# Performance work log

Hardware: AMD Instinct MI355X
Metric: run time of the kernel (lower is better)

## Reference

```python
import jax, jax.numpy as jnp
import numpy as np
from jax import lax

# ---- module config (matches init_kwargs) ----
TARGET_H, TARGET_W = 1024, 1024
SMOOTH_K = 3
DIL_K = 3
DIL_ITERS = 2
DIL_BETA = 5.0
DIL_STRENGTH = 1.0


def _cubic_weights(t):
    """Keys cubic convolution weights (a=-0.75, torch bicubic). t: [N] frac in [0,1). -> [N,4] for taps at offsets -1,0,1,2."""
    a = -0.75
    t1 = t + 1.0  # distance of tap -1
    w0 = a * t1**3 - 5.0 * a * t1**2 + 8.0 * a * t1 - 4.0 * a
    w1 = (a + 2.0) * t**3 - (a + 3.0) * t**2 + 1.0
    u = 1.0 - t
    w2 = (a + 2.0) * u**3 - (a + 3.0) * u**2 + 1.0
    u2 = 2.0 - t
    w3 = a * u2**3 - 5.0 * a * u2**2 + 8.0 * a * u2 - 4.0 * a
    return jnp.stack([w0, w1, w2, w3], axis=-1)


def _taps(n_in, n_out):
    # grid_sample with align_corners=True over a full linspace(-1,1) grid maps
    # output pixel j -> input coord linspace(0, n_in-1, n_out)[j]
    src = jnp.linspace(0.0, n_in - 1.0, n_out)
    i0 = jnp.floor(src)
    t = src - i0
    idx = (i0[:, None] + jnp.arange(-1, 3)[None, :]).astype(jnp.int32)
    idx = jnp.clip(idx, 0, n_in - 1)  # padding_mode='border'
    return idx, _cubic_weights(t)


def _resize_bicubic(x, ht, wt):
    B, C, H, W = x.shape
    ih, wh = _taps(H, ht)
    iw, ww = _taps(W, wt)
    # rows: [B,C,ht,4,W] -> weighted sum over taps
    xr = x[:, :, ih, :]
    xr = jnp.einsum('bcthw,th->bctw', xr.transpose(0, 1, 2, 4, 3), wh) if False else (xr * wh[None, None, :, :, None]).sum(axis=3)
    # cols: [B,C,ht,wt,4]
    xc = xr[:, :, :, iw]
    return (xc * ww[None, None, None, :, :]).sum(axis=-1)


def _gaussian_kernel(k):
    sigma = k / 3.0
    r = np.arange(k, dtype=np.float32) - k // 2
    k1 = np.exp(-0.5 * (r / sigma) ** 2)
    k1 = k1 / k1.sum()
    k2 = np.outer(k1, k1)
    return jnp.asarray(k2.reshape(1, 1, k, k))


def _smooth(x):
    kern = _gaussian_kernel(SMOOTH_K)
    pad = SMOOTH_K // 2
    return lax.conv_general_dilated(
        x, kern, window_strides=(1, 1), padding=[(pad, pad), (pad, pad)],
        dimension_numbers=('NCHW', 'OIHW', 'NCHW'))


def _soft_dilate(x):
    # windowed logsumexp: lse = (1/beta) * log sum_window exp(beta * x),
    # with zero padding inside the window (matches F.unfold padding).
    p = DIL_K // 2
    for _ in range(DIL_ITERS):
        xp = jnp.pad(x, ((0, 0), (0, 0), (p, p), (p, p)))
        e = jnp.exp(DIL_BETA * (xp - 1.0))  # shift by 1.0 (x in [0,1]) for stability
        s = lax.reduce_window(e, 0.0, lax.add, (1, 1, DIL_K, DIL_K), (1, 1, 1, 1), 'VALID')
        x = jnp.clip(1.0 + jnp.log(s) / DIL_BETA, 0.0, 1.0)
    return x  # DIL_STRENGTH == 1.0 -> no blend with original


def setup_inputs() -> dict:
    key = jax.random.key(0)
    detris_output = jax.random.normal(key, (8, 1, 256, 256), dtype=jnp.float32)
    return {"detris_output": detris_output}


def reference(detris_output) -> jnp.ndarray:
    x = jax.nn.sigmoid(detris_output)
    x = _resize_bicubic(x, TARGET_H, TARGET_W)
    x = _smooth(x)
    x = _soft_dilate(x)
    return x
```

## Files before the change

kernel.cpp:

```cpp
#include <hip/hip_runtime.h>
#include <hip/hip_fp16.h>

#define B_ 8
#define HI 256
#define WI 256
#define HO 1024
#define WO 1024

#define TLE 64
#define NRS 24
#define SSTR 25
#define HS 18
#define EW 38
#define SC (255.0f / 1023.0f)
#define F5L2E 7.2134752f
#define EXPM5 0.0067379470f
#define GW0 0.27406862f
#define GW1 0.45186276f
#define C02 0.13862944f

__device__ __forceinline__ int basef(int g) {
    int yc = min(max(g, 0), HO - 1);
    return (int)floorf((float)yc * SC) - 2;
}

__device__ __forceinline__ void tap6(int g, int* base_out, float w[6]) {
    int yc = min(max(g, 0), HO - 1);
    int base = basef(g);
#pragma unroll
    for (int s = 0; s < 6; ++s) w[s] = 0.0f;
    if (g >= 0 && g < HO) {
#pragma unroll
        for (int d = -1; d <= 1; ++d) {
            int yd = yc + d;
            if (yd < 0 || yd >= HO) continue;
            float src = (float)yd * SC;
            float fi0 = floorf(src);
            float tt = src - fi0;
            const float a = -0.75f;
            float t1 = tt + 1.0f;
            float c0 = ((a * t1 - 5.0f * a) * t1 + 8.0f * a) * t1 - 4.0f * a;
            float c1 = ((a + 2.0f) * tt - (a + 3.0f)) * tt * tt + 1.0f;
            float u = 1.0f - tt;
            float c2 = ((a + 2.0f) * u - (a + 3.0f)) * u * u + 1.0f;
            float u2 = 2.0f - tt;
            float c3 = ((a * u2 - 5.0f * a) * u2 + 8.0f * a) * u2 - 4.0f * a;
            int s0 = ((int)fi0 - 1) - base;
            float gg = (d == 0) ? GW1 : GW0;
            w[s0 + 0] += gg * c0;
            w[s0 + 1] += gg * c1;
            w[s0 + 2] += gg * c2;
            w[s0 + 3] += gg * c3;
        }
    }
    *base_out = base;
}

__device__ __forceinline__ void pad8(const float w[6], int d, float scl, float w8[8]) {
#pragma unroll
    for (int j = 0; j < 8; ++j) {
        float a = (j < 6) ? w[j] : 0.0f;
        float bq = (j >= 1 && j < 7) ? w[j - 1] : 0.0f;
        w8[j] = ((d == 0) ? a : bq) * scl;
    }
}

__device__ __forceinline__ __half2 hmin2(__half2 a, __half2 b) {
    unsigned int ua = __builtin_bit_cast(unsigned int, a);
    unsigned int ub = __builtin_bit_cast(unsigned int, b);
    unsigned int r;
    asm("v_pk_min_f16 %0, %1, %2" : "=v"(r) : "v"(ua), "v"(ub));
    return __builtin_bit_cast(__half2, r);
}

__global__ __launch_bounds__(256, 7) void k_fused(const float* __restrict__ in,
                                                  float* __restrict__ out) {
    __shared__ __align__(16) unsigned int Eu[68 * EW];
    __shared__ float4 Hs[NRS * HS];
    __shared__ float4 xAw[72], xBw[72];
    __shared__ float4 vAw[70], vBw[70];
    __shared__ int vgb[14], xgb[18];
    float* SL = (float*)Eu;

    const int tid = threadIdx.x;
    const int bx = blockIdx.x, by = blockIdx.y, b = blockIdx.z;
    const int gy0 = by * TLE, gx0 = bx * TLE;
    const int rlo = basef(gy0 - 3);
    const int clo = basef(gx0 - 4);

    const float* pin = in + b * (HI * WI);
    float g0, g1, g2 = 0.0f;
    {
        int i0 = tid, i1 = tid + 256;
        int r0 = i0 / NRS, c0 = i0 - r0 * NRS;
        int r1 = i1 / NRS, c1 = i1 - r1 * NRS;
        g0 = pin[min(max(rlo + r0, 0), HI - 1) * WI + min(max(clo + c0, 0), HI - 1)];
        g1 = pin[min(max(rlo + r1, 0), HI - 1) * WI + min(max(clo + c1, 0), HI - 1)];
        if (tid < 64) {
            int i2 = tid + 512;
            int r2 = i2 / NRS, c2 = i2 - r2 * NRS;
            g2 = pin[min(max(rlo + r2, 0), HI - 1) * WI + min(max(clo + c2, 0), HI - 1)];
        }
    }

    if (tid < 70) {
        int fy = tid + 1;
        int base; float w[6];
        tap6(gy0 + fy - 3, &base, w);
        int q = tid / 5;
        int bs = basef(gy0 + (1 + 5 * q) - 3);
        float w8[8];
        pad8(w, base - bs, F5L2E, w8);
        vAw[tid] = make_float4(w8[0], w8[1], w8[2], w8[3]);
        vBw[tid] = make_float4(w8[4], w8[5], w8[6], w8[7]);
    } else if (tid < 84) {
        vgb[tid - 70] = basef(gy0 + (1 + 5 * (tid - 70)) - 3);
    } else if (tid < 102) {
        xgb[tid - 84] = basef(gx0 + 4 * (tid - 84) - 4);
    } else if (tid >= 128 && tid < 200) {
        int xe = tid - 128;
        int base; float w[6];
        tap6(gx0 + xe - 4, &base, w);
        int bs = basef(gx0 + (xe & ~3) - 4);
        float w8[8];
        pad8(w, base - bs, 1.0f, w8);
        xAw[xe] = make_float4(w8[0], w8[1], w8[2], w8[3]);
        xBw[xe] = make_float4(w8[4], w8[5], w8[6], w8[7]);
    }

    {
        int i0 = tid, i1 = tid + 256;
        int r0 = i0 / NRS, c0 = i0 - r0 * NRS;
        int r1 = i1 / NRS, c1 = i1 - r1 * NRS;
        SL[r0 * SSTR + c0] = 1.0f / (1.0f + __expf(-g0));
        SL[r1 * SSTR + c1] = 1.0f / (1.0f + __expf(-g1));
        if (tid < 64) {
            int i2 = tid + 512;
            int r2 = i2 / NRS, c2 = i2 - r2 * NRS;
            SL[r2 * SSTR + c2] = 1.0f / (1.0f + __expf(-g2));
        }
    }
    __syncthreads();

    const int ty = tid / HS;
    const int tx = tid - ty * HS;

    if (tid < 252) {
        int cbg = xgb[tx] - clo;
        int wc[8];
#pragma unroll
        for (int j = 0; j < 8; ++j) wc[j] = min(cbg + j, NRS - 1);
        float xw0[8], xw1[8], xw2[8], xw3[8];
        {
            int xe0 = tx << 2;
            float4 a0 = xAw[xe0 + 0], b0 = xBw[xe0 + 0];
            float4 a1 = xAw[xe0 + 1], b1 = xBw[xe0 + 1];
            float4 a2 = xAw[xe0 + 2], b2 = xBw[xe0 + 2];
            float4 a3 = xAw[xe0 + 3], b3 = xBw[xe0 + 3];
            xw0[0]=a0.x; xw0[1]=a0.y; xw0[2]=a0.z; xw0[3]=a0.w; xw0[4]=b0.x; xw0[5]=b0.y; xw0[6]=b0.z; xw0[7]=b0.w;
            xw1[0]=a1.x; xw1[1]=a1.y; xw1[2]=a1.z; xw1[3]=a1.w; xw1[4]=b1.x; xw1[5]=b1.y; xw1[6]=b1.z; xw1[7]=b1.w;
            xw2[0]=a2.x; xw2[1]=a2.y; xw2[2]=a2.z; xw2[3]=a2.w; xw2[4]=b2.x; xw2[5]=b2.y; xw2[6]=b2.z; xw2[7]=b2.w;
            xw3[0]=a3.x; xw3[1]=a3.y; xw3[2]=a3.z; xw3[3]=a3.w; xw3[4]=b3.x; xw3[5]=b3.y; xw3[6]=b3.z; xw3[7]=b3.w;
        }
        for (int r = ty; r < NRS; r += 14) {
            const float* srow = SL + r * SSTR;
            float wnd[8];
#pragma unroll
            for (int j = 0; j < 8; ++j) wnd[j] = srow[wc[j]];
            float s0 = wnd[0]*xw0[0], s1 = wnd[0]*xw1[0], s2 = wnd[0]*xw2[0], s3 = wnd[0]*xw3[0];
#pragma unroll
            for (int j = 1; j < 8; ++j) {
                s0 = fmaf(wnd[j], xw0[j], s0);
                s1 = fmaf(wnd[j], xw1[j], s1);
                s2 = fmaf(wnd[j], xw2[j], s2);
                s3 = fmaf(wnd[j], xw3[j], s3);
            }
            Hs[r * HS + tx] = make_float4(s0, s1, s2, s3);
        }
    }
    __syncthreads();

    if (tid < 252) {
        const int q = ty;
        const int rbase = vgb[q] - rlo;
        float4 h[8];
#pragma unroll
        for (int i = 0; i < 8; ++i) h[i] = Hs[min(rbase + i, NRS - 1) * HS + tx];
#pragma unroll
        for (int i = 0; i < 5; ++i) {
            int fy = 1 + 5 * q + i;
            if (fy <= 68) {
                float4 wa = vAw[fy - 1], wb = vBw[fy - 1];
                const float wv[8] = {wa.x, wa.y, wa.z, wa.w, wb.x, wb.y, wb.z, wb.w};
                float ax = -F5L2E, ay = -F5L2E, az = -F5L2E, aw = -F5L2E;
#pragma unroll
                for (int j = 0; j < 8; ++j) {
                    ax = fmaf(wv[j], h[j].x, ax);
                    ay = fmaf(wv[j], h[j].y, ay);
                    az = fmaf(wv[j], h[j].z, az);
                    aw = fmaf(wv[j], h[j].w, aw);
                }
                unsigned int p0 = __builtin_bit_cast(unsigned int, __floats2half2_rn(exp2f(ax), exp2f(ay)));
                unsigned int p1 = __builtin_bit_cast(unsigned int, __floats2half2_rn(exp2f(az), exp2f(aw)));
                *reinterpret_cast<uint2*>(&Eu[(fy - 1) * EW + 2 * tx]) = make_uint2(p0, p1);
            }
        }
    }
    __syncthreads();

    {
        const int dx = tid & 15;
        const int sq = tid >> 4;
        const int lr0 = 4 * sq;
        const bool rT = (by == 0)  && (sq == 0);
        const bool rB = (by == 15) && (sq == 15);
        const bool cL = (bx == 0)  && (dx == 0);
        const bool cR = (bx == 15) && (dx == 15);

        const __half2 ONE2 = __floats2half2_rn(1.0f, 1.0f);
        const __half2 EX2  = __floats2half2_rn(EXPM5, EXPM5);
        const unsigned int exu = __builtin_bit_cast(unsigned int, EX2);

        auto H2  = [](unsigned int u) { return __builtin_bit_cast(__half2, u); };
        auto U32 = [](__half2 h) { return __builtin_bit_cast(unsigned int, h); };

        auto HSUM = [&](int lr, __half2 P[3]) {
            const int o = lr * EW + 2 * dx;
            unsigned int a = Eu[o + 1];
            uint2 bc = *reinterpret_cast<const uint2*>(&Eu[o + 2]);
            unsigned int d = Eu[o + 4];
            unsigned int ab  = (a >> 16) | (bc.x << 16);
            unsigned int bcx = (bc.x >> 16) | (bc.y << 16);
            unsigned int cd  = (bc.y >> 16) | (d << 16);
            P[0] = __hadd2(__hadd2(H2(a), H2(ab)), H2(bc.x));
            P[1] = __hadd2(__hadd2(H2(bc.x), H2(bcx)), H2(bc.y));
            P[2] = __hadd2(__hadd2(H2(bc.y), H2(cd)), H2(d));
        };
        auto E2F = [&](const __half2* a, const __half2* bq, const __half2* c,
                       bool rowOv, __half2 Q[2]) {
            __half2 e0 = hmin2(__hadd2(__hadd2(a[0], bq[0]), c[0]), ONE2);
            __half2 e1 = hmin2(__hadd2(__hadd2(a[1], bq[1]), c[1]), ONE2);
            __half2 e2 = hmin2(__hadd2(__hadd2(a[2], bq[2]), c[2]), ONE2);
            if (rowOv) { e0 = EX2; e1 = EX2; e2 = EX2; }
            if (cL) e0 = H2((U32(e0) & 0xFFFF0000u) | (exu & 0x0000FFFFu));
            if (cR) e2 = H2((U32(e2) & 0x0000FFFFu) | (exu & 0xFFFF0000u));
            unsigned int u0 = U32(e0), u1 = U32(e1), u2 = U32(e2);
            unsigned int e01 = (u0 >> 16) | (u1 << 16);
            unsigned int e12 = (u1 >> 16) | (u2 << 16);
            Q[0] = __hadd2(__hadd2(e0, H2(e01)), e1);
            Q[1] = __hadd2(__hadd2(e1, H2(e12)), e2);
        };
        auto OUTF = [&](const __half2* qa, const __half2* qb, const __half2* qc) -> float4 {
            __half2 s0 = __hadd2(__hadd2(qa[0], qb[0]), qc[0]);
            __half2 s1 = __hadd2(__hadd2(qa[1], qb[1]), qc[1]);
            float f0 = __low2float(s0), f1 = __high2float(s0);
            float f2 = __low2float(s1), f3 = __high2float(s1);
            float4 o;
            o.x = fmaxf(fminf(fmaf(C02, __log2f(f0), 1.0f), 1.0f), 0.0f);
            o.y = fmaxf(fminf(fmaf(C02, __log2f(f1), 1.0f), 1.0f), 0.0f);
            o.z = fmaxf(fminf(fmaf(C02, __log2f(f2), 1.0f), 1.0f), 0.0f);
            o.w = fmaxf(fminf(fmaf(C02, __log2f(f3), 1.0f), 1.0f), 0.0f);
            return o;
        };

        __half2 hA[3], hB[3], hC[3], hD[3];
        __half2 eA[2], eB[2], eC[2], eD[2], eE[2], eF[2];
        size_t obase = ((size_t)(b * HO + by * TLE + 4 * sq) * WO) + bx * TLE + (dx << 2);

        HSUM(lr0 + 0, hA); HSUM(lr0 + 1, hB); HSUM(lr0 + 2, hC);
        E2F(hA, hB, hC, rT, eA);
        HSUM(lr0 + 3, hD); E2F(hB, hC, hD, false, eB);
        HSUM(lr0 + 4, hA); E2F(hC, hD, hA, false, eC);
        *reinterpret_cast<float4*>(out + obase) = OUTF(eA, eB, eC); obase += WO;
        HSUM(lr0 + 5, hB); E2F(hD, hA, hB, false, eD);
        *reinterpret_cast<float4*>(out + obase) = OUTF(eB, eC, eD); obase += WO;
        HSUM(lr0 + 6, hC); E2F(hA, hB, hC, false, eE);
        *reinterpret_cast<float4*>(out + obase) = OUTF(eC, eD, eE); obase += WO;
        HSUM(lr0 + 7, hD); E2F(hB, hC, hD, rB, eF);
        *reinterpret_cast<float4*>(out + obase) = OUTF(eD, eE, eF);
    }
}

extern "C" void kernel_launch(void* const* d_in, const int* in_sizes, int n_in,
                              void* d_out, int out_size, void* d_ws, size_t ws_size,
                              hipStream_t stream) {
    const float* in = (const float*)d_in[0];
    float* out = (float*)d_out;
    dim3 g(WO / TLE, HO / TLE, B_);
    k_fused<<<g, dim3(256), 0, stream>>>(in, out);
}
```

Before: 23.35 us.

## Use packed fp16 dot2 for horizontal and vertical resize passes

Converts the resize weights and the intermediate horizontal-pass results to packed fp16 and computes both separable resize passes with v_dot2 fp16 instructions accumulating in fp32. This halves the shared-memory footprint of the weight tables and the intermediate buffer and cuts the FMA count roughly in half. The cost is extra pack and convert instructions and reduced precision of inputs and weights, which could affect accuracy. The exp argument is scaled by about 7.2, which amplifies fp16 rounding.

```diff
diff --git a/kernel.cpp b/kernel.cpp
--- a/kernel.cpp
+++ b/kernel.cpp
@@ -10,7 +10,6 @@
 #define TLE 64
 #define NRS 24
 #define SSTR 25
-#define HS 18
 #define EW 38
 #define SC (255.0f / 1023.0f)
 #define F5L2E 7.2134752f
@@ -18,6 +17,13 @@
 #define GW0 0.27406862f
 #define GW1 0.45186276f
 #define C02 0.13862944f
+
+typedef _Float16 f16x2 __attribute__((ext_vector_type(2)));
+
+__device__ __forceinline__ float dot2(unsigned int a, unsigned int b, float c) {
+    return __builtin_amdgcn_fdot2(__builtin_bit_cast(f16x2, a),
+                                  __builtin_bit_cast(f16x2, b), c, false);
+}
 
 __device__ __forceinline__ int basef(int g) {
     int yc = min(max(g, 0), HO - 1);
@@ -65,6 +71,15 @@
     }
 }
 
+__device__ __forceinline__ uint4 packw8(const float w8[8]) {
+    uint4 r;
+    r.x = __builtin_bit_cast(unsigned int, __floats2half2_rn(w8[0], w8[1]));
+    r.y = __builtin_bit_cast(unsigned int, __floats2half2_rn(w8[2], w8[3]));
+    r.z = __builtin_bit_cast(unsigned int, __floats2half2_rn(w8[4], w8[5]));
+    r.w = __builtin_bit_cast(unsigned int, __floats2half2_rn(w8[6], w8[7]));
+    return r;
+}
+
 __device__ __forceinline__ __half2 hmin2(__half2 a, __half2 b) {
     unsigned int ua = __builtin_bit_cast(unsigned int, a);
     unsigned int ub = __builtin_bit_cast(unsigned int, b);
@@ -76,9 +91,9 @@
 __global__ __launch_bounds__(256, 7) void k_fused(const float* __restrict__ in,
                                                   float* __restrict__ out) {
     __shared__ __align__(16) unsigned int Eu[68 * EW];
-    __shared__ float4 Hs[NRS * HS];
-    __shared__ float4 xAw[72], xBw[72];
-    __shared__ float4 vAw[70], vBw[70];
+    __shared__ __align__(16) unsigned int Hu[NRS * EW];
+    __shared__ uint4 xWu[72];
+    __shared__ uint4 vWu[70];
     __shared__ int vgb[14], xgb[18];
     float* SL = (float*)Eu;
 
@@ -111,8 +126,7 @@
         int bs = basef(gy0 + (1 + 5 * q) - 3);
         float w8[8];
         pad8(w, base - bs, F5L2E, w8);
-        vAw[tid] = make_float4(w8[0], w8[1], w8[2], w8[3]);
-        vBw[tid] = make_float4(w8[4], w8[5], w8[6], w8[7]);
+        vWu[tid] = packw8(w8);
     } else if (tid < 84) {
         vgb[tid - 70] = basef(gy0 + (1 + 5 * (tid - 70)) - 3);
     } else if (tid < 102) {
@@ -124,8 +138,7 @@
         int bs = basef(gx0 + (xe & ~3) - 4);
         float w8[8];
         pad8(w, base - bs, 1.0f, w8);
-        xAw[xe] = make_float4(w8[0], w8[1], w8[2], w8[3]);
-        xBw[xe] = make_float4(w8[4], w8[5], w8[6], w8[7]);
+        xWu[xe] = packw8(w8);
     }
 
     {
@@ -142,40 +155,33 @@
     }
     __syncthreads();
 
-    const int ty = tid / HS;
-    const int tx = tid - ty * HS;
+    const int ty = tid / 18;
+    const int tx = tid - ty * 18;
 
     if (tid < 252) {
         int cbg = xgb[tx] - clo;
         int wc[8];
 #pragma unroll
         for (int j = 0; j < 8; ++j) wc[j] = min(cbg + j, NRS - 1);
-        float xw0[8], xw1[8], xw2[8], xw3[8];
-        {
-            int xe0 = tx << 2;
-            float4 a0 = xAw[xe0 + 0], b0 = xBw[xe0 + 0];
-            float4 a1 = xAw[xe0 + 1], b1 = xBw[xe0 + 1];
-            float4 a2 = xAw[xe0 + 2], b2 = xBw[xe0 + 2];
-            float4 a3 = xAw[xe0 + 3], b3 = xBw[xe0 + 3];
-            xw0[0]=a0.x; xw0[1]=a0.y; xw0[2]=a0.z; xw0[3]=a0.w; xw0[4]=b0.x; xw0[5]=b0.y; xw0[6]=b0.z; xw0[7]=b0.w;
-            xw1[0]=a1.x; xw1[1]=a1.y; xw1[2]=a1.z; xw1[3]=a1.w; xw1[4]=b1.x; xw1[5]=b1.y; xw1[6]=b1.z; xw1[7]=b1.w;
-            xw2[0]=a2.x; xw2[1]=a2.y; xw2[2]=a2.z; xw2[3]=a2.w; xw2[4]=b2.x; xw2[5]=b2.y; xw2[6]=b2.z; xw2[7]=b2.w;
-            xw3[0]=a3.x; xw3[1]=a3.y; xw3[2]=a3.z; xw3[3]=a3.w; xw3[4]=b3.x; xw3[5]=b3.y; xw3[6]=b3.z; xw3[7]=b3.w;
-        }
+        uint4 w0 = xWu[4 * tx + 0], w1 = xWu[4 * tx + 1];
+        uint4 w2 = xWu[4 * tx + 2], w3 = xWu[4 * tx + 3];
         for (int r = ty; r < NRS; r += 14) {
             const float* srow = SL + r * SSTR;
-            float wnd[8];
-#pragma unroll
-            for (int j = 0; j < 8; ++j) wnd[j] = srow[wc[j]];
-            float s0 = wnd[0]*xw0[0], s1 = wnd[0]*xw1[0], s2 = wnd[0]*xw2[0], s3 = wnd[0]*xw3[0];
-#pragma unroll
-            for (int j = 1; j < 8; ++j) {
-                s0 = fmaf(wnd[j], xw0[j], s0);
-                s1 = fmaf(wnd[j], xw1[j], s1);
-                s2 = fmaf(wnd[j], xw2[j], s2);
-                s3 = fmaf(wnd[j], xw3[j], s3);
-            }
-            Hs[r * HS + tx] = make_float4(s0, s1, s2, s3);
+            float v[8];
+#pragma unroll
+            for (int j = 0; j < 8; ++j) v[j] = srow[wc[j]];
+            unsigned int p0 = __builtin_bit_cast(unsigned int, __floats2half2_rn(v[0], v[1]));
+            unsigned int p1 = __builtin_bit_cast(unsigned int, __floats2half2_rn(v[2], v[3]));
+            unsigned int p2 = __builtin_bit_cast(unsigned int, __floats2half2_rn(v[4], v[5]));
+            unsigned int p3 = __builtin_bit_cast(unsigned int, __floats2half2_rn(v[6], v[7]));
+            float s0 = dot2(w0.x, p0, dot2(w0.y, p1, dot2(w0.z, p2, dot2(w0.w, p3, 0.0f))));
+            float s1 = dot2(w1.x, p0, dot2(w1.y, p1, dot2(w1.z, p2, dot2(w1.w, p3, 0.0f))));
+            float s2 = dot2(w2.x, p0, dot2(w2.y, p1, dot2(w2.z, p2, dot2(w2.w, p3, 0.0f))));
+            float s3 = dot2(w3.x, p0, dot2(w3.y, p1, dot2(w3.z, p2, dot2(w3.w, p3, 0.0f))));
+            uint2 o;
+            o.x = __builtin_bit_cast(unsigned int, __floats2half2_rn(s0, s1));
+            o.y = __builtin_bit_cast(unsigned int, __floats2half2_rn(s2, s3));
+            *reinterpret_cast<uint2*>(&Hu[r * EW + 2 * tx]) = o;
         }
     }
     __syncthreads();
@@ -183,23 +189,30 @@
     if (tid < 252) {
         const int q = ty;
         const int rbase = vgb[q] - rlo;
-        float4 h[8];
-#pragma unroll
-        for (int i = 0; i < 8; ++i) h[i] = Hs[min(rbase + i, NRS - 1) * HS + tx];
+        unsigned int a01[8], a23[8];
+#pragma unroll
+        for (int i = 0; i < 8; ++i) {
+            uint2 t = *reinterpret_cast<const uint2*>(&Hu[min(rbase + i, NRS - 1) * EW + 2 * tx]);
+            a01[i] = t.x; a23[i] = t.y;
+        }
+        unsigned int pc0[4], pc1[4], pc2[4], pc3[4];
+#pragma unroll
+        for (int p = 0; p < 4; ++p) {
+            int j = 2 * p;
+            pc0[p] = (a01[j] & 0xFFFFu) | (a01[j + 1] << 16);
+            pc1[p] = (a01[j] >> 16) | (a01[j + 1] & 0xFFFF0000u);
+            pc2[p] = (a23[j] & 0xFFFFu) | (a23[j + 1] << 16);
+            pc3[p] = (a23[j] >> 16) | (a23[j + 1] & 0xFFFF0000u);
+        }
 #pragma unroll
         for (int i = 0; i < 5; ++i) {
             int fy = 1 + 5 * q + i;
             if (fy <= 68) {
-                float4 wa = vAw[fy - 1], wb = vBw[fy - 1];
-                const float wv[8] = {wa.x, wa.y, wa.z, wa.w, wb.x, wb.y, wb.z, wb.w};
-                float ax = -F5L2E, ay = -F5L2E, az = -F5L2E, aw = -F5L2E;
-#pragma unroll
-                for (int j = 0; j < 8; ++j) {
-                    ax = fmaf(wv[j], h[j].x, ax);
-                    ay = fmaf(wv[j], h[j].y, ay);
-                    az = fmaf(wv[j], h[j].z, az);
-                    aw = fmaf(wv[j], h[j].w, aw);
-                }
+                uint4 wv = vWu[fy - 1];
+                float ax = dot2(wv.x, pc0[0], dot2(wv.y, pc0[1], dot2(wv.z, pc0[2], dot2(wv.w, pc0[3], -F5L2E))));
+                float ay = dot2(wv.x, pc1[0], dot2(wv.y, pc1[1], dot2(wv.z, pc1[2], dot2(wv.w, pc1[3], -F5L2E))));
+                float az = dot2(wv.x, pc2[0], dot2(wv.y, pc2[1], dot2(wv.z, pc2[2], dot2(wv.w, pc2[3], -F5L2E))));
+                float aw = dot2(wv.x, pc3[0], dot2(wv.y, pc3[1], dot2(wv.z, pc3[2], dot2(wv.w, pc3[3], -F5L2E))));
                 unsigned int p0 = __builtin_bit_cast(unsigned int, __floats2half2_rn(exp2f(ax), exp2f(ay)));
                 unsigned int p1 = __builtin_bit_cast(unsigned int, __floats2half2_rn(exp2f(az), exp2f(aw)));
                 *reinterpret_cast<uint2*>(&Eu[(fy - 1) * EW + 2 * tx]) = make_uint2(p0, p1);
```

After: 23.27 us. No clear change (-0.3%).
